# Kernel optimization log

Hardware: AMD Instinct MI355X
Metric: run time of the kernel (lower is better)

Reference implementation:

```python
import jax, jax.numpy as jnp
import numpy as np

D_MODEL = 768
HEADS = 12
D_K = D_MODEL // HEADS
NEG = -1e9


def setup_inputs() -> dict:
    key = jax.random.key(0)
    ks = jax.random.split(key, 7)
    B, S, D = 4, 2048, D_MODEL
    scale = 1.0 / np.sqrt(D)
    q = jax.random.normal(ks[0], (B, S, D), dtype=jnp.float32)
    k = jax.random.normal(ks[1], (B, S, D), dtype=jnp.float32)
    v = jax.random.normal(ks[2], (B, S, D), dtype=jnp.float32)
    # causal mask, broadcastable over batch and heads; mask==0 -> -1e9
    mask = jnp.tril(jnp.ones((1, 1, S, S), dtype=jnp.int32))
    W_q = jax.random.normal(ks[3], (D, D), dtype=jnp.float32) * scale
    W_k = jax.random.normal(ks[4], (D, D), dtype=jnp.float32) * scale
    W_v = jax.random.normal(ks[5], (D, D), dtype=jnp.float32) * scale
    W_o = jax.random.normal(ks[6], (D, D), dtype=jnp.float32) * scale
    return {"q": q, "k": k, "v": v, "mask": mask,
            "W_q": W_q, "W_k": W_k, "W_v": W_v, "W_o": W_o}


def reference(q, k, v, mask, W_q, W_k, W_v, W_o):
    B, S, D = q.shape
    # nn.Linear(bias=False): y = x @ W.T
    query = (q @ W_q.T).reshape(B, S, HEADS, D_K).transpose(0, 2, 1, 3)  # [B,H,S,dk]
    key_ = (k @ W_k.T).reshape(B, S, HEADS, D_K).transpose(0, 2, 1, 3)
    value = (v @ W_v.T).reshape(B, S, HEADS, D_K).transpose(0, 2, 1, 3)
    scores = jnp.einsum('bhqd,bhkd->bhqk', query, key_) / jnp.sqrt(
        jnp.asarray(D_K, dtype=query.dtype))
    scores = jnp.where(mask == 0, jnp.asarray(NEG, dtype=scores.dtype), scores)
    attn = jax.nn.softmax(scores, axis=-1)
    # dropout rate = 0.0 (inference / eval mode): identity
    x = jnp.einsum('bhqk,bhkd->bhqd', attn, value)  # [B,H,S,dk]
    x = x.transpose(0, 2, 1, 3).reshape(B, S, D)
    return x @ W_o.T
```

## Files before the change

kernel.cpp:

```cpp
#include <hip/hip_runtime.h>


typedef _Float16 f16x8 __attribute__((ext_vector_type(8)));
typedef _Float16 f16x4 __attribute__((ext_vector_type(4)));
typedef float floatx4 __attribute__((ext_vector_type(4)));

#define MFMA16(a, b, c) __builtin_amdgcn_mfma_f32_16x16x32_f16((a), (b), (c), 0, 0, 0)

static constexpr int B_ = 4;
static constexpr int S_ = 2048;
static constexpr int D_ = 768;
static constexpr int H_ = 12;
static constexpr int DK = 64;

__device__ __forceinline__ f16x8 cvt8(float4 a, float4 b) {
  f16x8 h;
  h[0] = (_Float16)a.x; h[1] = (_Float16)a.y;
  h[2] = (_Float16)a.z; h[3] = (_Float16)a.w;
  h[4] = (_Float16)b.x; h[5] = (_Float16)b.y;
  h[6] = (_Float16)b.z; h[7] = (_Float16)b.w;
  return h;
}

__device__ __forceinline__ void dma16(const _Float16* g, _Float16* l) {
  __builtin_amdgcn_global_load_lds(
      (const __attribute__((address_space(1))) unsigned int*)g,
      (__attribute__((address_space(3))) unsigned int*)l, 16, 0, 0);
}

struct CvtArgs {
  const float* src[7];
  _Float16* dst[7];
  int end[7];
  int nseg;
};

__global__ __launch_bounds__(256) void cvt_f32_f16(CvtArgs a) {
  int b = blockIdx.x;
  int s = 0;
  while (s < a.nseg - 1 && b >= a.end[s]) ++s;
  int local = b - (s ? a.end[s - 1] : 0);
  const int tid = threadIdx.x;
  const float4* p = (const float4*)(a.src[s] + (size_t)local * 2048) + tid * 2;
  float4 x0 = p[0], x1 = p[1];
  *(f16x8*)(a.dst[s] + (size_t)local * 2048 + tid * 8) = cvt8(x0, x1);
}

struct QkvPtrs {
  const void* a[3];
  const void* w[3];
};

template <int AP, int BP>
__global__ __launch_bounds__(256) void qkv_gemm(QkvPtrs P, _Float16* Qh,
                                                _Float16* Kh, _Float16* Vt) {
  constexpr int SA = AP ? 32 : 40;
  constexpr int SB = BP ? 32 : 40;
  constexpr int K = 768;
  __shared__ _Float16 As[128 * 40];
  __shared__ _Float16 Bs[128 * 40];

  const int z = blockIdx.z;
  const void* Av = P.a[z];
  const void* Bv = P.w[z];

  const int tid = threadIdx.x;
  const int wave = tid >> 6, lane = tid & 63;
  const int l15 = lane & 15, quad = lane >> 4;
  const int wm = (wave >> 1) * 64, wn = (wave & 1) * 64;
  const int m0 = blockIdx.y * 128, n0 = blockIdx.x * 128;

  const int srow = tid >> 1, scol = (tid & 1) * 16;
  const int c0 = wave * 64 + lane, c1 = 256 + wave * 64 + lane;
  const int r0 = c0 >> 2, cc0 = (c0 & 3) * 8;
  const int r1 = c1 >> 2, cc1 = (c1 & 3) * 8;

  floatx4 acc[4][4] = {};

  for (int k0 = 0; k0 < K; k0 += 32) {
    if constexpr (AP == 1) {
      const _Float16* A = (const _Float16*)Av;
      dma16(A + (size_t)(m0 + r0) * K + k0 + cc0, As + wave * 64 * 8);
      dma16(A + (size_t)(m0 + r1) * K + k0 + cc1, As + (256 + wave * 64) * 8);
    } else {
      const float* A = (const float*)Av;
      const float4* p = (const float4*)(A + (size_t)(m0 + srow) * K + k0 + scol);
      float4 x0 = p[0], x1 = p[1], x2 = p[2], x3 = p[3];
      *(f16x8*)(As + srow * 40 + scol) = cvt8(x0, x1);
      *(f16x8*)(As + srow * 40 + scol + 8) = cvt8(x2, x3);
    }
    if constexpr (BP == 1) {
      const _Float16* Bp = (const _Float16*)Bv;
      dma16(Bp + (size_t)(n0 + r0) * K + k0 + cc0, Bs + wave * 64 * 8);
      dma16(Bp + (size_t)(n0 + r1) * K + k0 + cc1, Bs + (256 + wave * 64) * 8);
    } else {
      const float* Bp = (const float*)Bv;
      const float4* p =
          (const float4*)(Bp + (size_t)(n0 + srow) * K + k0 + scol);
      float4 x0 = p[0], x1 = p[1], x2 = p[2], x3 = p[3];
      *(f16x8*)(Bs + srow * 40 + scol) = cvt8(x0, x1);
      *(f16x8*)(Bs + srow * 40 + scol + 8) = cvt8(x2, x3);
    }
    __syncthreads();

    f16x8 af[4], bf[4];
#pragma unroll
    for (int t = 0; t < 4; ++t)
      af[t] = *(const f16x8*)(As + (wm + t * 16 + l15) * SA + quad * 8);
#pragma unroll
    for (int t = 0; t < 4; ++t)
      bf[t] = *(const f16x8*)(Bs + (wn + t * 16 + l15) * SB + quad * 8);
#pragma unroll
    for (int mt = 0; mt < 4; ++mt)
#pragma unroll
      for (int nt = 0; nt < 4; ++nt)
        acc[mt][nt] = MFMA16(af[mt], bf[nt], acc[mt][nt]);
    __syncthreads();
  }

  const float scale = (z == 0) ? 0.125f : 1.0f;
  if (z < 2) {
    _Float16* C = z ? Kh : Qh;
#pragma unroll
    for (int mt = 0; mt < 4; ++mt)
#pragma unroll
      for (int nt = 0; nt < 4; ++nt)
#pragma unroll
        for (int r = 0; r < 4; ++r) {
          int row = m0 + wm + mt * 16 + quad * 4 + r;
          int col = n0 + wn + nt * 16 + l15;
          int b = row >> 11, s = row & 2047;
          int h = col >> 6, d = col & 63;
          C[((size_t)(b * H_ + h) * S_ + s) * DK + d] =
              (_Float16)(acc[mt][nt][r] * scale);
        }
  } else {
#pragma unroll
    for (int mt = 0; mt < 4; ++mt)
#pragma unroll
      for (int nt = 0; nt < 4; ++nt) {
        int row = m0 + wm + mt * 16 + quad * 4;
        int col = n0 + wn + nt * 16 + l15;
        int b = row >> 11, s = row & 2047;
        int h = col >> 6, d = col & 63;
        f16x4 v4;
#pragma unroll
        for (int r = 0; r < 4; ++r) v4[r] = (_Float16)acc[mt][nt][r];
        *(f16x4*)(Vt + ((size_t)(b * H_ + h) * DK + d) * S_ + s) = v4;
      }
  }
}

template <int AP, int BP, int MODE, bool SCALE>
__global__ __launch_bounds__(256) void gemm128(const void* __restrict__ Av,
                                               const void* __restrict__ Bv,
                                               void* __restrict__ Cv,
                                               int M, int N, int K) {
  constexpr int SA = AP ? 32 : 40;
  constexpr int SB = BP ? 32 : 40;
  __shared__ _Float16 As[128 * 40];
  __shared__ _Float16 Bs[128 * 40];

  const int tid = threadIdx.x;
  const int wave = tid >> 6, lane = tid & 63;
  const int l15 = lane & 15, quad = lane >> 4;
  const int wm = (wave >> 1) * 64, wn = (wave & 1) * 64;
  const int m0 = blockIdx.y * 128, n0 = blockIdx.x * 128;

  const int srow = tid >> 1, scol = (tid & 1) * 16;
  const int c0 = wave * 64 + lane, c1 = 256 + wave * 64 + lane;
  const int r0 = c0 >> 2, cc0 = (c0 & 3) * 8;
  const int r1 = c1 >> 2, cc1 = (c1 & 3) * 8;

  floatx4 acc[4][4] = {};

  for (int k0 = 0; k0 < K; k0 += 32) {
    if constexpr (AP == 1) {
      const _Float16* A = (const _Float16*)Av;
      dma16(A + (size_t)(m0 + r0) * K + k0 + cc0, As + wave * 64 * 8);
      dma16(A + (size_t)(m0 + r1) * K + k0 + cc1, As + (256 + wave * 64) * 8);
    } else {
      const float* A = (const float*)Av;
      const float4* p = (const float4*)(A + (size_t)(m0 + srow) * K + k0 + scol);
      float4 x0 = p[0], x1 = p[1], x2 = p[2], x3 = p[3];
      *(f16x8*)(As + srow * 40 + scol) = cvt8(x0, x1);
      *(f16x8*)(As + srow * 40 + scol + 8) = cvt8(x2, x3);
    }
    if constexpr (BP == 1) {
      const _Float16* Bp = (const _Float16*)Bv;
      dma16(Bp + (size_t)(n0 + r0) * K + k0 + cc0, Bs + wave * 64 * 8);
      dma16(Bp + (size_t)(n0 + r1) * K + k0 + cc1, Bs + (256 + wave * 64) * 8);
    } else {
      const float* Bp = (const float*)Bv;
      const float4* p =
          (const float4*)(Bp + (size_t)(n0 + srow) * K + k0 + scol);
      float4 x0 = p[0], x1 = p[1], x2 = p[2], x3 = p[3];
      *(f16x8*)(Bs + srow * 40 + scol) = cvt8(x0, x1);
      *(f16x8*)(Bs + srow * 40 + scol + 8) = cvt8(x2, x3);
    }
    __syncthreads();

    f16x8 af[4], bf[4];
#pragma unroll
    for (int t = 0; t < 4; ++t)
      af[t] = *(const f16x8*)(As + (wm + t * 16 + l15) * SA + quad * 8);
#pragma unroll
    for (int t = 0; t < 4; ++t)
      bf[t] = *(const f16x8*)(Bs + (wn + t * 16 + l15) * SB + quad * 8);
#pragma unroll
    for (int mt = 0; mt < 4; ++mt)
#pragma unroll
      for (int nt = 0; nt < 4; ++nt)
        acc[mt][nt] = MFMA16(af[mt], bf[nt], acc[mt][nt]);
    __syncthreads();
  }

#pragma unroll
  for (int mt = 0; mt < 4; ++mt)
#pragma unroll
    for (int nt = 0; nt < 4; ++nt)
#pragma unroll
      for (int r = 0; r < 4; ++r) {
        int row = m0 + wm + mt * 16 + quad * 4 + r;
        int col = n0 + wn + nt * 16 + l15;
        float val = acc[mt][nt][r];
        if constexpr (SCALE) val *= 0.125f;
        if constexpr (MODE == 0) {
          ((float*)Cv)[(size_t)row * N + col] = val;
        } else if constexpr (MODE == 1) {
          int b = row >> 11, s = row & 2047;
          int h = col >> 6, d = col & 63;
          ((_Float16*)Cv)[((size_t)(b * H_ + h) * S_ + s) * DK + d] =
              (_Float16)val;
        } else {
          int b = col >> 11, s = col & 2047;
          int h = row >> 6, d = row & 63;
          ((_Float16*)Cv)[((size_t)(b * H_ + h) * DK + d) * S_ + s] =
              (_Float16)val;
        }
      }
}

__global__ __launch_bounds__(256, 4) void flash_attn(
    const _Float16* __restrict__ Qh, const _Float16* __restrict__ Kh,
    const _Float16* __restrict__ Vt, _Float16* __restrict__ Oh) {
  __shared__ _Float16 Ks[64 * 72];
  __shared__ _Float16 Vts[64 * 72];
  __shared__ _Float16 Ps[4][16 * 36];

  const int tid = threadIdx.x;
  const int wave = tid >> 6, lane = tid & 63;
  const int l15 = lane & 15, quad = lane >> 4;

  const int linear = blockIdx.x + gridDim.x * blockIdx.y;
  const int xcd = linear & 7;
  const int seq = linear >> 3;
  const int bh = xcd * 6 + (seq >> 4);
  const int xp = seq & 15;
  const int b = bh / H_, h = bh % H_;
  const size_t base = (size_t)bh * S_ * DK;
  const size_t basev = (size_t)bh * DK * S_;

  const int srow = tid >> 2;
  const int sc0 = (tid & 3) * 16;

  for (int c = 0; c < 2; ++c) {
    const int qt = c ? xp : 31 - xp;
    const int q0 = qt * 64;
    const int qrow = q0 + wave * 16 + l15;
    f16x8 qf0 = *(const f16x8*)(Qh + base + (size_t)qrow * DK + quad * 8);
    f16x8 qf1 = *(const f16x8*)(Qh + base + (size_t)qrow * DK + 32 + quad * 8);

    floatx4 o_acc[4] = {};
    float plsum[4] = {0.f, 0.f, 0.f, 0.f};

    const _Float16* ks = Kh + base + (size_t)srow * DK + sc0;
    const _Float16* vs = Vt + basev + (size_t)srow * S_ + sc0;
    f16x8 pk0 = *(const f16x8*)ks;
    f16x8 pk1 = *(const f16x8*)(ks + 8);
    f16x8 pv0 = *(const f16x8*)vs;
    f16x8 pv1 = *(const f16x8*)(vs + 8);

    for (int j = 0; j <= qt; ++j) {
      __syncthreads();
      *(f16x8*)(Ks + srow * 72 + sc0) = pk0;
      *(f16x8*)(Ks + srow * 72 + sc0 + 8) = pk1;
      *(f16x8*)(Vts + srow * 72 + sc0) = pv0;
      *(f16x8*)(Vts + srow * 72 + sc0 + 8) = pv1;
      __syncthreads();

      if (j < qt) {
        const _Float16* kn =
            Kh + base + (size_t)((j + 1) * 64 + srow) * DK + sc0;
        const _Float16* vn =
            Vt + basev + (size_t)srow * S_ + (j + 1) * 64 + sc0;
        pk0 = *(const f16x8*)kn;
        pk1 = *(const f16x8*)(kn + 8);
        pv0 = *(const f16x8*)vn;
        pv1 = *(const f16x8*)(vn + 8);
      }

      floatx4 s_acc[4] = {};
#pragma unroll
      for (int t = 0; t < 4; ++t) {
        f16x8 kf0 = *(const f16x8*)(Ks + (t * 16 + l15) * 72 + quad * 8);
        f16x8 kf1 = *(const f16x8*)(Ks + (t * 16 + l15) * 72 + 32 + quad * 8);
        s_acc[t] = MFMA16(qf0, kf0, s_acc[t]);
        s_acc[t] = MFMA16(qf1, kf1, s_acc[t]);
      }

      const bool diag = (j == qt);
      const int j0 = j * 64;
      float p[4][4];
#pragma unroll
      for (int t = 0; t < 4; ++t)
#pragma unroll
        for (int r = 0; r < 4; ++r) {
          float s = s_acc[t][r];
          if (diag) {
            int rg = q0 + wave * 16 + quad * 4 + r;
            int cg = j0 + t * 16 + l15;
            if (cg > rg) s = -1e30f;
          }
          float e = __expf(s);
          p[t][r] = e;
          plsum[r] += e;
        }

#pragma unroll
      for (int t = 0; t < 2; ++t)
#pragma unroll
        for (int r = 0; r < 4; ++r)
          Ps[wave][(quad * 4 + r) * 36 + t * 16 + l15] = (_Float16)p[t][r];
      f16x8 pf0 = *(const f16x8*)(Ps[wave] + l15 * 36 + quad * 8);
#pragma unroll
      for (int t = 0; t < 4; ++t) {
        f16x8 vf0 = *(const f16x8*)(Vts + (t * 16 + l15) * 72 + quad * 8);
        o_acc[t] = MFMA16(pf0, vf0, o_acc[t]);
      }
#pragma unroll
      for (int t = 2; t < 4; ++t)
#pragma unroll
        for (int r = 0; r < 4; ++r)
          Ps[wave][(quad * 4 + r) * 36 + (t - 2) * 16 + l15] =
              (_Float16)p[t][r];
      f16x8 pf1 = *(const f16x8*)(Ps[wave] + l15 * 36 + quad * 8);
#pragma unroll
      for (int t = 0; t < 4; ++t) {
        f16x8 vf1 = *(const f16x8*)(Vts + (t * 16 + l15) * 72 + 32 + quad * 8);
        o_acc[t] = MFMA16(pf1, vf1, o_acc[t]);
      }
    }

#pragma unroll
    for (int r = 0; r < 4; ++r) {
      float l = plsum[r];
      l += __shfl_xor(l, 1);
      l += __shfl_xor(l, 2);
      l += __shfl_xor(l, 4);
      l += __shfl_xor(l, 8);
      float inv = 1.0f / l;
      int row = q0 + wave * 16 + quad * 4 + r;
#pragma unroll
      for (int t = 0; t < 4; ++t) {
        float val = o_acc[t][r] * inv;
        Oh[((size_t)(b * S_ + row)) * D_ + h * DK + t * 16 + l15] =
            (_Float16)val;
      }
    }
  }
}

extern "C" void kernel_launch(void* const* d_in, const int* in_sizes, int n_in,
                              void* d_out, int out_size, void* d_ws,
                              size_t ws_size, hipStream_t stream) {
  const float* q = (const float*)d_in[0];
  const float* k = (const float*)d_in[1];
  const float* v = (const float*)d_in[2];
  const float* Wq = (const float*)d_in[4];
  const float* Wk = (const float*)d_in[5];
  const float* Wv = (const float*)d_in[6];
  const float* Wo = (const float*)d_in[7];
  float* out = (float*)d_out;

  const size_t E = (size_t)B_ * H_ * S_ * DK;
  const size_t EW = (size_t)D_ * D_;
  _Float16* Qh = (_Float16*)d_ws;
  _Float16* Kh = Qh + E;
  _Float16* Vt = Kh + E;
  _Float16* Oh = Vt + E;

  const int M = B_ * S_;
  dim3 blk(256);
  dim3 qg(D_ / 128, M / 128, 3);
  dim3 pg(D_ / 128, M / 128);
  dim3 fg(16, B_ * H_);

  const size_t need_full = (7 * E + 4 * EW) * 2;
  const size_t need_w = (4 * E + 4 * EW) * 2;

  if (ws_size >= need_full) {
    _Float16* qf = Oh + E;
    _Float16* kf = qf + E;
    _Float16* vf = kf + E;
    _Float16* wqf = vf + E;
    _Float16* wkf = wqf + EW;
    _Float16* wvf = wkf + EW;
    _Float16* wof = wvf + EW;
    CvtArgs ca;
    ca.src[0] = q;  ca.dst[0] = qf;
    ca.src[1] = k;  ca.dst[1] = kf;
    ca.src[2] = v;  ca.dst[2] = vf;
    ca.src[3] = Wq; ca.dst[3] = wqf;
    ca.src[4] = Wk; ca.dst[4] = wkf;
    ca.src[5] = Wv; ca.dst[5] = wvf;
    ca.src[6] = Wo; ca.dst[6] = wof;
    int ends[7] = {3072, 6144, 9216, 9504, 9792, 10080, 10368};
    for (int i = 0; i < 7; ++i) ca.end[i] = ends[i];
    ca.nseg = 7;
    cvt_f32_f16<<<10368, blk, 0, stream>>>(ca);
    QkvPtrs P;
    P.a[0] = qf; P.a[1] = kf; P.a[2] = vf;
    P.w[0] = wqf; P.w[1] = wkf; P.w[2] = wvf;
    qkv_gemm<1, 1><<<qg, blk, 0, stream>>>(P, Qh, Kh, Vt);
    flash_attn<<<fg, blk, 0, stream>>>(Qh, Kh, Vt, Oh);
    gemm128<1, 1, 0, false><<<pg, blk, 0, stream>>>(Oh, wof, out, M, D_, D_);
  } else if (ws_size >= need_w) {
    _Float16* wqf = Oh + E;
    _Float16* wkf = wqf + EW;
    _Float16* wvf = wkf + EW;
    _Float16* wof = wvf + EW;
    CvtArgs ca;
    ca.src[0] = Wq; ca.dst[0] = wqf;
    ca.src[1] = Wk; ca.dst[1] = wkf;
    ca.src[2] = Wv; ca.dst[2] = wvf;
    ca.src[3] = Wo; ca.dst[3] = wof;
    int ends[4] = {288, 576, 864, 1152};
    for (int i = 0; i < 4; ++i) ca.end[i] = ends[i];
    ca.nseg = 4;
    cvt_f32_f16<<<1152, blk, 0, stream>>>(ca);
    QkvPtrs P;
    P.a[0] = q; P.a[1] = k; P.a[2] = v;
    P.w[0] = wqf; P.w[1] = wkf; P.w[2] = wvf;
    qkv_gemm<0, 1><<<qg, blk, 0, stream>>>(P, Qh, Kh, Vt);
    flash_attn<<<fg, blk, 0, stream>>>(Qh, Kh, Vt, Oh);
    gemm128<1, 1, 0, false><<<pg, blk, 0, stream>>>(Oh, wof, out, M, D_, D_);
  } else {
    QkvPtrs P;
    P.a[0] = q; P.a[1] = k; P.a[2] = v;
    P.w[0] = Wq; P.w[1] = Wk; P.w[2] = Wv;
    qkv_gemm<0, 0><<<qg, blk, 0, stream>>>(P, Qh, Kh, Vt);
    flash_attn<<<fg, blk, 0, stream>>>(Qh, Kh, Vt, Oh);
    gemm128<1, 0, 0, false><<<pg, blk, 0, stream>>>(Oh, Wo, out, M, D_, D_);
  }
}
```

Baseline: 276.8 us.

## Drop full f16 pre-conversion path, restructure QKV/out GEMMs and flash attention tiling

```diff
diff --git a/kernel.cpp b/kernel.cpp
--- a/kernel.cpp
+++ b/kernel.cpp
@@ -29,9 +29,9 @@
 }
 
 struct CvtArgs {
-  const float* src[7];
-  _Float16* dst[7];
-  int end[7];
+  const float* src[4];
+  _Float16* dst[4];
+  int end[4];
   int nseg;
 };
 
@@ -46,75 +46,70 @@
   *(f16x8*)(a.dst[s] + (size_t)local * 2048 + tid * 8) = cvt8(x0, x1);
 }
 
+static constexpr int PAN = 128 * 32;
+
 struct QkvPtrs {
   const void* a[3];
   const void* w[3];
 };
 
-template <int AP, int BP>
-__global__ __launch_bounds__(256) void qkv_gemm(QkvPtrs P, _Float16* Qh,
+__global__ __launch_bounds__(256) void qkv_f32a(QkvPtrs P, _Float16* Qh,
                                                 _Float16* Kh, _Float16* Vt) {
-  constexpr int SA = AP ? 32 : 40;
-  constexpr int SB = BP ? 32 : 40;
+  __shared__ _Float16 As[2 * PAN];
+  __shared__ _Float16 Bs[2 * PAN];
   constexpr int K = 768;
-  __shared__ _Float16 As[128 * 40];
-  __shared__ _Float16 Bs[128 * 40];
 
   const int z = blockIdx.z;
-  const void* Av = P.a[z];
-  const void* Bv = P.w[z];
+  const float* A = (const float*)P.a[z];
+  const _Float16* W = (const _Float16*)P.w[z];
 
   const int tid = threadIdx.x;
   const int wave = tid >> 6, lane = tid & 63;
   const int l15 = lane & 15, quad = lane >> 4;
   const int wm = (wave >> 1) * 64, wn = (wave & 1) * 64;
   const int m0 = blockIdx.y * 128, n0 = blockIdx.x * 128;
-
-  const int srow = tid >> 1, scol = (tid & 1) * 16;
-  const int c0 = wave * 64 + lane, c1 = 256 + wave * 64 + lane;
-  const int r0 = c0 >> 2, cc0 = (c0 & 3) * 8;
-  const int r1 = c1 >> 2, cc1 = (c1 & 3) * 8;
+  const int lr = lane >> 2, lc = (lane & 3) * 8;
 
   floatx4 acc[4][4] = {};
 
-  for (int k0 = 0; k0 < K; k0 += 32) {
-    if constexpr (AP == 1) {
-      const _Float16* A = (const _Float16*)Av;
-      dma16(A + (size_t)(m0 + r0) * K + k0 + cc0, As + wave * 64 * 8);
-      dma16(A + (size_t)(m0 + r1) * K + k0 + cc1, As + (256 + wave * 64) * 8);
-    } else {
-      const float* A = (const float*)Av;
-      const float4* p = (const float4*)(A + (size_t)(m0 + srow) * K + k0 + scol);
-      float4 x0 = p[0], x1 = p[1], x2 = p[2], x3 = p[3];
-      *(f16x8*)(As + srow * 40 + scol) = cvt8(x0, x1);
-      *(f16x8*)(As + srow * 40 + scol + 8) = cvt8(x2, x3);
-    }
-    if constexpr (BP == 1) {
-      const _Float16* Bp = (const _Float16*)Bv;
-      dma16(Bp + (size_t)(n0 + r0) * K + k0 + cc0, Bs + wave * 64 * 8);
-      dma16(Bp + (size_t)(n0 + r1) * K + k0 + cc1, Bs + (256 + wave * 64) * 8);
-    } else {
-      const float* Bp = (const float*)Bv;
+  for (int k0 = 0; k0 < K; k0 += 64) {
+    {
+      const _Float16* g = W + (size_t)(n0 + wave * 16 + lr) * K + k0 + lc;
+      dma16(g, Bs + wave * 16 * 32);
+      dma16(g + 32, Bs + PAN + wave * 16 * 32);
+      const _Float16* g2 = g + (size_t)64 * K;
+      dma16(g2, Bs + (64 + wave * 16) * 32);
+      dma16(g2 + 32, Bs + PAN + (64 + wave * 16) * 32);
+    }
+#pragma unroll
+    for (int jj = 0; jj < 4; ++jj) {
+      int flat8 = jj * 256 + tid;
+      int row = flat8 >> 3;
+      int k8 = flat8 & 7;
       const float4* p =
-          (const float4*)(Bp + (size_t)(n0 + srow) * K + k0 + scol);
-      float4 x0 = p[0], x1 = p[1], x2 = p[2], x3 = p[3];
-      *(f16x8*)(Bs + srow * 40 + scol) = cvt8(x0, x1);
-      *(f16x8*)(Bs + srow * 40 + scol + 8) = cvt8(x2, x3);
-    }
-    __syncthreads();
-
-    f16x8 af[4], bf[4];
-#pragma unroll
-    for (int t = 0; t < 4; ++t)
-      af[t] = *(const f16x8*)(As + (wm + t * 16 + l15) * SA + quad * 8);
-#pragma unroll
-    for (int t = 0; t < 4; ++t)
-      bf[t] = *(const f16x8*)(Bs + (wn + t * 16 + l15) * SB + quad * 8);
-#pragma unroll
-    for (int mt = 0; mt < 4; ++mt)
-#pragma unroll
-      for (int nt = 0; nt < 4; ++nt)
-        acc[mt][nt] = MFMA16(af[mt], bf[nt], acc[mt][nt]);
+          (const float4*)(A + (size_t)(m0 + row) * K + k0 + k8 * 8);
+      float4 x0 = p[0], x1 = p[1];
+      *(f16x8*)(As + (k8 >> 2) * PAN + row * 32 + (k8 & 3) * 8) = cvt8(x0, x1);
+    }
+    __syncthreads();
+
+#pragma unroll
+    for (int p = 0; p < 2; ++p) {
+      f16x8 af[4], bf[4];
+#pragma unroll
+      for (int t = 0; t < 4; ++t)
+        af[t] = *(const f16x8*)(As + p * PAN + (wm + t * 16 + l15) * 32 +
+                                quad * 8);
+#pragma unroll
+      for (int t = 0; t < 4; ++t)
+        bf[t] = *(const f16x8*)(Bs + p * PAN + (wn + t * 16 + l15) * 32 +
+                                quad * 8);
+#pragma unroll
+      for (int mt = 0; mt < 4; ++mt)
+#pragma unroll
+        for (int nt = 0; nt < 4; ++nt)
+          acc[mt][nt] = MFMA16(af[mt], bf[nt], acc[mt][nt]);
+    }
     __syncthreads();
   }
 
@@ -151,13 +146,80 @@
   }
 }
 
-template <int AP, int BP, int MODE, bool SCALE>
-__global__ __launch_bounds__(256) void gemm128(const void* __restrict__ Av,
-                                               const void* __restrict__ Bv,
-                                               void* __restrict__ Cv,
-                                               int M, int N, int K) {
-  constexpr int SA = AP ? 32 : 40;
-  constexpr int SB = BP ? 32 : 40;
+static constexpr int PAN_A = 64 * 32;
+static constexpr int PAN_B = 128 * 32;
+
+__global__ __launch_bounds__(256) void gemm_o64(const _Float16* __restrict__ A,
+                                                const _Float16* __restrict__ W,
+                                                float* __restrict__ C) {
+  __shared__ _Float16 As[2 * PAN_A];
+  __shared__ _Float16 Bs[2 * PAN_B];
+  constexpr int K = 768;
+  constexpr int N = 768;
+
+  const int tid = threadIdx.x;
+  const int wave = tid >> 6, lane = tid & 63;
+  const int l15 = lane & 15, quad = lane >> 4;
+  const int wm = (wave >> 1) * 32, wn = (wave & 1) * 64;
+  const int m0 = blockIdx.y * 64, n0 = blockIdx.x * 128;
+  const int lr = lane >> 2, lc = (lane & 3) * 8;
+
+  floatx4 acc[2][4] = {};
+
+  for (int k0 = 0; k0 < K; k0 += 64) {
+#pragma unroll
+    for (int p = 0; p < 2; ++p) {
+      const _Float16* g =
+          A + (size_t)(m0 + wave * 16 + lr) * K + k0 + p * 32 + lc;
+      dma16(g, As + p * PAN_A + wave * 16 * 32);
+    }
+#pragma unroll
+    for (int p = 0; p < 2; ++p)
+#pragma unroll
+      for (int q = 0; q < 2; ++q) {
+        const _Float16* g =
+            W + (size_t)(n0 + wave * 32 + q * 16 + lr) * K + k0 + p * 32 + lc;
+        dma16(g, Bs + p * PAN_B + (wave * 32 + q * 16) * 32);
+      }
+    __syncthreads();
+
+#pragma unroll
+    for (int p = 0; p < 2; ++p) {
+      f16x8 af[2], bf[4];
+#pragma unroll
+      for (int t = 0; t < 2; ++t)
+        af[t] = *(const f16x8*)(As + p * PAN_A + (wm + t * 16 + l15) * 32 +
+                                quad * 8);
+#pragma unroll
+      for (int t = 0; t < 4; ++t)
+        bf[t] = *(const f16x8*)(Bs + p * PAN_B + (wn + t * 16 + l15) * 32 +
+                                quad * 8);
+#pragma unroll
+      for (int mt = 0; mt < 2; ++mt)
+#pragma unroll
+        for (int nt = 0; nt < 4; ++nt)
+          acc[mt][nt] = MFMA16(af[mt], bf[nt], acc[mt][nt]);
+    }
+    __syncthreads();
+  }
+
+#pragma unroll
+  for (int mt = 0; mt < 2; ++mt)
+#pragma unroll
+    for (int nt = 0; nt < 4; ++nt)
+#pragma unroll
+      for (int r = 0; r < 4; ++r) {
+        int row = m0 + wm + mt * 16 + quad * 4 + r;
+        int col = n0 + wn + nt * 16 + l15;
+        C[(size_t)row * N + col] = acc[mt][nt][r];
+      }
+}
+
+template <int MODE, bool SCALE>
+__global__ __launch_bounds__(256) void gemm128(const float* __restrict__ Av,
+                                               const float* __restrict__ Bv,
+                                               void* __restrict__ Cv, int M,
+                                               int N, int K) {
   __shared__ _Float16 As[128 * 40];
   __shared__ _Float16 Bs[128 * 40];
 
@@ -166,34 +228,21 @@
   const int l15 = lane & 15, quad = lane >> 4;
   const int wm = (wave >> 1) * 64, wn = (wave & 1) * 64;
   const int m0 = blockIdx.y * 128, n0 = blockIdx.x * 128;
-
   const int srow = tid >> 1, scol = (tid & 1) * 16;
-  const int c0 = wave * 64 + lane, c1 = 256 + wave * 64 + lane;
-  const int r0 = c0 >> 2, cc0 = (c0 & 3) * 8;
-  const int r1 = c1 >> 2, cc1 = (c1 & 3) * 8;
 
   floatx4 acc[4][4] = {};
 
   for (int k0 = 0; k0 < K; k0 += 32) {
-    if constexpr (AP == 1) {
-      const _Float16* A = (const _Float16*)Av;
-      dma16(A + (size_t)(m0 + r0) * K + k0 + cc0, As + wave * 64 * 8);
-      dma16(A + (size_t)(m0 + r1) * K + k0 + cc1, As + (256 + wave * 64) * 8);
-    } else {
-      const float* A = (const float*)Av;
-      const float4* p = (const float4*)(A + (size_t)(m0 + srow) * K + k0 + scol);
+    {
+      const float4* p =
+          (const float4*)(Av + (size_t)(m0 + srow) * K + k0 + scol);
       float4 x0 = p[0], x1 = p[1], x2 = p[2], x3 = p[3];
       *(f16x8*)(As + srow * 40 + scol) = cvt8(x0, x1);
       *(f16x8*)(As + srow * 40 + scol + 8) = cvt8(x2, x3);
     }
-    if constexpr (BP == 1) {
-      const _Float16* Bp = (const _Float16*)Bv;
-      dma16(Bp + (size_t)(n0 + r0) * K + k0 + cc0, Bs + wave * 64 * 8);
-      dma16(Bp + (size_t)(n0 + r1) * K + k0 + cc1, Bs + (256 + wave * 64) * 8);
-    } else {
-      const float* Bp = (const float*)Bv;
+    {
       const float4* p =
-          (const float4*)(Bp + (size_t)(n0 + srow) * K + k0 + scol);
+          (const float4*)(Bv + (size_t)(n0 + srow) * K + k0 + scol);
       float4 x0 = p[0], x1 = p[1], x2 = p[2], x3 = p[3];
       *(f16x8*)(Bs + srow * 40 + scol) = cvt8(x0, x1);
       *(f16x8*)(Bs + srow * 40 + scol + 8) = cvt8(x2, x3);
@@ -203,10 +252,10 @@
     f16x8 af[4], bf[4];
 #pragma unroll
     for (int t = 0; t < 4; ++t)
-      af[t] = *(const f16x8*)(As + (wm + t * 16 + l15) * SA + quad * 8);
+      af[t] = *(const f16x8*)(As + (wm + t * 16 + l15) * 40 + quad * 8);
 #pragma unroll
     for (int t = 0; t < 4; ++t)
-      bf[t] = *(const f16x8*)(Bs + (wn + t * 16 + l15) * SB + quad * 8);
+      bf[t] = *(const f16x8*)(Bs + (wn + t * 16 + l15) * 40 + quad * 8);
 #pragma unroll
     for (int mt = 0; mt < 4; ++mt)
 #pragma unroll
@@ -241,7 +290,65 @@
       }
 }
 
-__global__ __launch_bounds__(256, 4) void flash_attn(
+__global__ __launch_bounds__(256) void gemm_out_f32w(
+    const _Float16* __restrict__ A, const float* __restrict__ Bv,
+    float* __restrict__ C) {
+  __shared__ _Float16 As[128 * 40];
+  __shared__ _Float16 Bs[128 * 40];
+  constexpr int K = 768, N = 768;
+
+  const int tid = threadIdx.x;
+  const int wave = tid >> 6, lane = tid & 63;
+  const int l15 = lane & 15, quad = lane >> 4;
+  const int wm = (wave >> 1) * 64, wn = (wave & 1) * 64;
+  const int m0 = blockIdx.y * 128, n0 = blockIdx.x * 128;
+  const int srow = tid >> 1, scol = (tid & 1) * 16;
+
+  floatx4 acc[4][4] = {};
+
+  for (int k0 = 0; k0 < K; k0 += 32) {
+    {
+      const f16x8* p = (const f16x8*)(A + (size_t)(m0 + srow) * K + k0 + scol);
+      *(f16x8*)(As + srow * 40 + scol) = p[0];
+      *(f16x8*)(As + srow * 40 + scol + 8) = p[1];
+    }
+    {
+      const float4* p =
+          (const float4*)(Bv + (size_t)(n0 + srow) * K + k0 + scol);
+      float4 x0 = p[0], x1 = p[1], x2 = p[2], x3 = p[3];
+      *(f16x8*)(Bs + srow * 40 + scol) = cvt8(x0, x1);
+      *(f16x8*)(Bs + srow * 40 + scol + 8) = cvt8(x2, x3);
+    }
+    __syncthreads();
+
+    f16x8 af[4], bf[4];
+#pragma unroll
+    for (int t = 0; t < 4; ++t)
+      af[t] = *(const f16x8*)(As + (wm + t * 16 + l15) * 40 + quad * 8);
+#pragma unroll
+    for (int t = 0; t < 4; ++t)
+      bf[t] = *(const f16x8*)(Bs + (wn + t * 16 + l15) * 40 + quad * 8);
+#pragma unroll
+    for (int mt = 0; mt < 4; ++mt)
+#pragma unroll
+      for (int nt = 0; nt < 4; ++nt)
+        acc[mt][nt] = MFMA16(af[mt], bf[nt], acc[mt][nt]);
+    __syncthreads();
+  }
+
+#pragma unroll
+  for (int mt = 0; mt < 4; ++mt)
+#pragma unroll
+    for (int nt = 0; nt < 4; ++nt)
+#pragma unroll
+      for (int r = 0; r < 4; ++r) {
+        int row = m0 + wm + mt * 16 + quad * 4 + r;
+        int col = n0 + wn + nt * 16 + l15;
+        C[(size_t)row * N + col] = acc[mt][nt][r];
+      }
+}
+
+__global__ __launch_bounds__(256, 3) void flash_attn(
     const _Float16* __restrict__ Qh, const _Float16* __restrict__ Kh,
     const _Float16* __restrict__ Vt, _Float16* __restrict__ Oh) {
   __shared__ _Float16 Ks[64 * 72];
@@ -256,75 +363,81 @@
   const int xcd = linear & 7;
   const int seq = linear >> 3;
   const int bh = xcd * 6 + (seq >> 4);
-  const int xp = seq & 15;
+  const int qt = 15 - (seq & 15);
   const int b = bh / H_, h = bh % H_;
+  const int q0 = qt * 128;
   const size_t base = (size_t)bh * S_ * DK;
   const size_t basev = (size_t)bh * DK * S_;
 
+  f16x8 qf[2][2];
+#pragma unroll
+  for (int mt = 0; mt < 2; ++mt) {
+    int qrow = q0 + mt * 64 + wave * 16 + l15;
+    qf[mt][0] = *(const f16x8*)(Qh + base + (size_t)qrow * DK + quad * 8);
+    qf[mt][1] = *(const f16x8*)(Qh + base + (size_t)qrow * DK + 32 + quad * 8);
+  }
+
+  floatx4 o_acc[2][4] = {};
+  float plsum[2][4] = {};
+
   const int srow = tid >> 2;
   const int sc0 = (tid & 3) * 16;
-
-  for (int c = 0; c < 2; ++c) {
-    const int qt = c ? xp : 31 - xp;
-    const int q0 = qt * 64;
-    const int qrow = q0 + wave * 16 + l15;
-    f16x8 qf0 = *(const f16x8*)(Qh + base + (size_t)qrow * DK + quad * 8);
-    f16x8 qf1 = *(const f16x8*)(Qh + base + (size_t)qrow * DK + 32 + quad * 8);
-
-    floatx4 o_acc[4] = {};
-    float plsum[4] = {0.f, 0.f, 0.f, 0.f};
-
-    const _Float16* ks = Kh + base + (size_t)srow * DK + sc0;
-    const _Float16* vs = Vt + basev + (size_t)srow * S_ + sc0;
-    f16x8 pk0 = *(const f16x8*)ks;
-    f16x8 pk1 = *(const f16x8*)(ks + 8);
-    f16x8 pv0 = *(const f16x8*)vs;
-    f16x8 pv1 = *(const f16x8*)(vs + 8);
-
-    for (int j = 0; j <= qt; ++j) {
-      __syncthreads();
-      *(f16x8*)(Ks + srow * 72 + sc0) = pk0;
-      *(f16x8*)(Ks + srow * 72 + sc0 + 8) = pk1;
-      *(f16x8*)(Vts + srow * 72 + sc0) = pv0;
-      *(f16x8*)(Vts + srow * 72 + sc0 + 8) = pv1;
-      __syncthreads();
-
-      if (j < qt) {
-        const _Float16* kn =
-            Kh + base + (size_t)((j + 1) * 64 + srow) * DK + sc0;
-        const _Float16* vn =
-            Vt + basev + (size_t)srow * S_ + (j + 1) * 64 + sc0;
-        pk0 = *(const f16x8*)kn;
-        pk1 = *(const f16x8*)(kn + 8);
-        pv0 = *(const f16x8*)vn;
-        pv1 = *(const f16x8*)(vn + 8);
-      }
+  const int jmax = 2 * qt + 1;
+
+  const _Float16* ks = Kh + base + (size_t)srow * DK + sc0;
+  const _Float16* vs = Vt + basev + (size_t)srow * S_ + sc0;
+  f16x8 pk0 = *(const f16x8*)ks;
+  f16x8 pk1 = *(const f16x8*)(ks + 8);
+  f16x8 pv0 = *(const f16x8*)vs;
+  f16x8 pv1 = *(const f16x8*)(vs + 8);
+
+  for (int j = 0; j <= jmax; ++j) {
+    const int j0 = j * 64;
+    __syncthreads();
+    *(f16x8*)(Ks + srow * 72 + sc0) = pk0;
+    *(f16x8*)(Ks + srow * 72 + sc0 + 8) = pk1;
+    *(f16x8*)(Vts + srow * 72 + sc0) = pv0;
+    *(f16x8*)(Vts + srow * 72 + sc0 + 8) = pv1;
+    __syncthreads();
+
+    if (j < jmax) {
+      const _Float16* kn = Kh + base + (size_t)((j + 1) * 64 + srow) * DK + sc0;
+      const _Float16* vn = Vt + basev + (size_t)srow * S_ + (j + 1) * 64 + sc0;
+      pk0 = *(const f16x8*)kn;
+      pk1 = *(const f16x8*)(kn + 8);
+      pv0 = *(const f16x8*)vn;
+      pv1 = *(const f16x8*)(vn + 8);
+    }
+
+#pragma unroll
+    for (int mt = 0; mt < 2; ++mt) {
+      const int rbase = q0 + mt * 64 + wave * 16;
+      if (j0 > rbase + 15) continue;
 
       floatx4 s_acc[4] = {};
 #pragma unroll
       for (int t = 0; t < 4; ++t) {
         f16x8 kf0 = *(const f16x8*)(Ks + (t * 16 + l15) * 72 + quad * 8);
         f16x8 kf1 = *(const f16x8*)(Ks + (t * 16 + l15) * 72 + 32 + quad * 8);
-        s_acc[t] = MFMA16(qf0, kf0, s_acc[t]);
-        s_acc[t] = MFMA16(qf1, kf1, s_acc[t]);
-      }
-
-      const bool diag = (j == qt);
-      const int j0 = j * 64;
+        s_acc[t] = MFMA16(qf[mt][0], kf0, s_acc[t]);
+        s_acc[t] = MFMA16(qf[mt][1], kf1, s_acc[t]);
+      }
+
+      const bool need_mask = (j0 + 63 > rbase);
       float p[4][4];
 #pragma unroll
       for (int t = 0; t < 4; ++t)
 #pragma unroll
         for (int r = 0; r < 4; ++r) {
           float s = s_acc[t][r];
-          if (diag) {
-            int rg = q0 + wave * 16 + quad * 4 + r;
+          if (need_mask) {
+            int rg = rbase + quad * 4 + r;
             int cg = j0 + t * 16 + l15;
             if (cg > rg) s = -1e30f;
           }
           float e = __expf(s);
           p[t][r] = e;
-          plsum[r] += e;
+          plsum[mt][r] += e;
         }
 
 #pragma unroll
@@ -336,7 +449,7 @@
 #pragma unroll
       for (int t = 0; t < 4; ++t) {
         f16x8 vf0 = *(const f16x8*)(Vts + (t * 16 + l15) * 72 + quad * 8);
-        o_acc[t] = MFMA16(pf0, vf0, o_acc[t]);
+        o_acc[mt][t] = MFMA16(pf0, vf0, o_acc[mt][t]);
       }
 #pragma unroll
       for (int t = 2; t < 4; ++t)
@@ -348,27 +461,29 @@
 #pragma unroll
       for (int t = 0; t < 4; ++t) {
         f16x8 vf1 = *(const f16x8*)(Vts + (t * 16 + l15) * 72 + 32 + quad * 8);
-        o_acc[t] = MFMA16(pf1, vf1, o_acc[t]);
-      }
-    }
-
+        o_acc[mt][t] = MFMA16(pf1, vf1, o_acc[mt][t]);
+      }
+    }
+  }
+
+#pragma unroll
+  for (int mt = 0; mt < 2; ++mt)
 #pragma unroll
     for (int r = 0; r < 4; ++r) {
-      float l = plsum[r];
+      float l = plsum[mt][r];
       l += __shfl_xor(l, 1);
       l += __shfl_xor(l, 2);
       l += __shfl_xor(l, 4);
       l += __shfl_xor(l, 8);
       float inv = 1.0f / l;
-      int row = q0 + wave * 16 + quad * 4 + r;
+      int row = q0 + mt * 64 + wave * 16 + quad * 4 + r;
 #pragma unroll
       for (int t = 0; t < 4; ++t) {
-        float val = o_acc[t][r] * inv;
+        float val = o_acc[mt][t][r] * inv;
         Oh[((size_t)(b * S_ + row)) * D_ + h * DK + t * 16 + l15] =
             (_Float16)val;
       }
     }
-  }
 }
 
 extern "C" void kernel_launch(void* const* d_in, const int* in_sizes, int n_in,
@@ -393,39 +508,13 @@
   const int M = B_ * S_;
   dim3 blk(256);
   dim3 qg(D_ / 128, M / 128, 3);
+  dim3 og(D_ / 128, M / 64);
   dim3 pg(D_ / 128, M / 128);
   dim3 fg(16, B_ * H_);
 
-  const size_t need_full = (7 * E + 4 * EW) * 2;
   const size_t need_w = (4 * E + 4 * EW) * 2;
 
-  if (ws_size >= need_full) {
-    _Float16* qf = Oh + E;
-    _Float16* kf = qf + E;
-    _Float16* vf = kf + E;
-    _Float16* wqf = vf + E;
-    _Float16* wkf = wqf + EW;
-    _Float16* wvf = wkf + EW;
-    _Float16* wof = wvf + EW;
-    CvtArgs ca;
-    ca.src[0] = q;  ca.dst[0] = qf;
-    ca.src[1] = k;  ca.dst[1] = kf;
-    ca.src[2] = v;  ca.dst[2] = vf;
-    ca.src[3] = Wq; ca.dst[3] = wqf;
-    ca.src[4] = Wk; ca.dst[4] = wkf;
-    ca.src[5] = Wv; ca.dst[5] = wvf;
-    ca.src[6] = Wo; ca.dst[6] = wof;
-    int ends[7] = {3072, 6144, 9216, 9504, 9792, 10080, 10368};
-    for (int i = 0; i < 7; ++i) ca.end[i] = ends[i];
-    ca.nseg = 7;
-    cvt_f32_f16<<<10368, blk, 0, stream>>>(ca);
-    QkvPtrs P;
-    P.a[0] = qf; P.a[1] = kf; P.a[2] = vf;
-    P.w[0] = wqf; P.w[1] = wkf; P.w[2] = wvf;
-    qkv_gemm<1, 1><<<qg, blk, 0, stream>>>(P, Qh, Kh, Vt);
-    flash_attn<<<fg, blk, 0, stream>>>(Qh, Kh, Vt, Oh);
-    gemm128<1, 1, 0, false><<<pg, blk, 0, stream>>>(Oh, wof, out, M, D_, D_);
-  } else if (ws_size >= need_w) {
+  if (ws_size >= need_w) {
     _Float16* wqf = Oh + E;
     _Float16* wkf = wqf + EW;
     _Float16* wvf = wkf + EW;
@@ -442,15 +531,15 @@
     QkvPtrs P;
     P.a[0] = q; P.a[1] = k; P.a[2] = v;
     P.w[0] = wqf; P.w[1] = wkf; P.w[2] = wvf;
-    qkv_gemm<0, 1><<<qg, blk, 0, stream>>>(P, Qh, Kh, Vt);
+    qkv_f32a<<<qg, blk, 0, stream>>>(P, Qh, Kh, Vt);
     flash_attn<<<fg, blk, 0, stream>>>(Qh, Kh, Vt, Oh);
-    gemm128<1, 1, 0, false><<<pg, blk, 0, stream>>>(Oh, wof, out, M, D_, D_);
+    gemm_o64<<<og, blk, 0, stream>>>(Oh, wof, out);
   } else {
-    QkvPtrs P;
-    P.a[0] = q; P.a[1] = k; P.a[2] = v;
-    P.w[0] = Wq; P.w[1] = Wk; P.w[2] = Wv;
-    qkv_gemm<0, 0><<<qg, blk, 0, stream>>>(P, Qh, Kh, Vt);
+    gemm128<1, true><<<pg, blk, 0, stream>>>(q, Wq, Qh, M, D_, D_);
+    gemm128<1, false><<<pg, blk, 0, stream>>>(k, Wk, Kh, M, D_, D_);
+    gemm128<2, false><<<dim3(M / 128, D_ / 128), blk, 0, stream>>>(
+        Wv, v, Vt, D_, M, D_);
     flash_attn<<<fg, blk, 0, stream>>>(Qh, Kh, Vt, Oh);
-    gemm128<1, 0, 0, false><<<pg, blk, 0, stream>>>(Oh, Wo, out, M, D_, D_);
-  }
-}
+    gemm_out_f32w<<<pg, blk, 0, stream>>>(Oh, Wo, out);
+  }
+}
```

New measurement: 304.7 us. 1.1x slower.
